# Optimization experiments

Hardware: AMD Instinct MI355X
Metric: run time of the kernel (lower is better)

The kernel has to match this reference:

```python
import jax, jax.numpy as jnp
import numpy as np

H = 64  # hidden size (fixed by module)

def _gru_cell(x, h, Wih, Whh, bih, bhh):
    # PyTorch GRU cell: gates ordered (r, z, n)
    gi = x @ Wih.T + bih            # [B, 3H]
    gh = h @ Whh.T + bhh            # [B, 3H]
    ir, iz, inn = jnp.split(gi, 3, axis=-1)
    hr, hz, hn = jnp.split(gh, 3, axis=-1)
    r = jax.nn.sigmoid(ir + hr)
    z = jax.nn.sigmoid(iz + hz)
    n = jnp.tanh(inn + r * hn)
    return (1.0 - z) * n + z * h


def setup_inputs() -> dict:
    key = jax.random.key(0)
    ks = jax.random.split(key, 24)
    B, T, NI = 16384, 256, 6
    s = 1.0 / np.sqrt(H)  # torch default GRU init scale
    f32 = jnp.float32
    u = lambda k, shp: jax.random.uniform(k, shp, dtype=f32, minval=-s, maxval=s)
    inp = {
        "x": jax.random.normal(ks[0], (B, T, NI), dtype=f32),
        "target_len": 180,
        # encoder GRU, layer 0 (input size NI) and layer 1 (input size H)
        "e_Wih0": u(ks[1], (3 * H, NI)), "e_Whh0": u(ks[2], (3 * H, H)),
        "e_bih0": u(ks[3], (3 * H,)),    "e_bhh0": u(ks[4], (3 * H,)),
        "e_Wih1": u(ks[5], (3 * H, H)),  "e_Whh1": u(ks[6], (3 * H, H)),
        "e_bih1": u(ks[7], (3 * H,)),    "e_bhh1": u(ks[8], (3 * H,)),
        # decoder GRU, layer 0 (input size 1) and layer 1 (input size H)
        "d_Wih0": u(ks[9], (3 * H, 1)),  "d_Whh0": u(ks[10], (3 * H, H)),
        "d_bih0": u(ks[11], (3 * H,)),   "d_bhh0": u(ks[12], (3 * H,)),
        "d_Wih1": u(ks[13], (3 * H, H)), "d_Whh1": u(ks[14], (3 * H, H)),
        "d_bih1": u(ks[15], (3 * H,)),   "d_bhh1": u(ks[16], (3 * H,)),
        # heads
        "W_on": u(ks[17], (1, H)), "b_on": u(ks[18], (1,)),
        "W_cv": u(ks[19], (1, H)), "b_cv": u(ks[20], (1,)),
    }
    return inp


def reference(x, target_len,
              e_Wih0, e_Whh0, e_bih0, e_bhh0, e_Wih1, e_Whh1, e_bih1, e_bhh1,
              d_Wih0, d_Whh0, d_bih0, d_bhh0, d_Wih1, d_Whh1, d_bih1, d_bhh1,
              W_on, b_on, W_cv, b_cv):
    B = x.shape[0]
    on_threshold = 0.5

    # ---- encoder: 2-layer GRU over the input sequence, keep final hidden ----
    def enc_step(carry, xt):
        h0, h1 = carry
        h0 = _gru_cell(xt, h0, e_Wih0, e_Whh0, e_bih0, e_bhh0)
        h1 = _gru_cell(h0, h1, e_Wih1, e_Whh1, e_bih1, e_bhh1)
        return (h0, h1), None

    h_init = (jnp.zeros((B, H), x.dtype), jnp.zeros((B, H), x.dtype))
    (h0, h1), _ = jax.lax.scan(enc_step, h_init, jnp.swapaxes(x, 0, 1))  # [T,B,NI]

    def dec_step(carry, _):
        prev, h0, h1 = carry                                   # prev: [B,1]
        h0 = _gru_cell(prev, h0, d_Wih0, d_Whh0, d_bih0, d_bhh0)
        h1 = _gru_cell(h0, h1, d_Wih1, d_Whh1, d_bih1, d_bhh1)
        cv = h1 @ W_cv.T + b_cv                                # [B,1]
        logit = h1 @ W_on.T + b_on                             # [B,1]
        gated = (jax.nn.sigmoid(logit) > on_threshold).astype(cv.dtype) * cv
        return (gated, h0, h1), gated

    prev0 = jnp.zeros((B, 1), x.dtype)
    _, outs = jax.lax.scan(dec_step, (prev0, h0, h1), None, length=target_len)
    # outs: [target_len, B, 1] -> [B, target_len, 1] (torch.cat along dim=1)
    return jnp.swapaxes(outs, 0, 1)
```

## Files before the change

### kernel.cpp

```cpp
#include <hip/hip_runtime.h>
#include <math.h>

#define TENC 256
#define NIE  6
#define LH   68
#define WSTR 68

__shared__ float sW1[192 * WSTR];
__shared__ float sU1[192 * WSTR];
__shared__ float sHd[132];
__shared__ float sh0[64 * LH];
__shared__ float sh1[64 * LH];

__device__ __forceinline__ float sigm_(float x) { return 1.0f / (1.0f + expf(-x)); }

__device__ __forceinline__ void fma4(float& acc, const float4& a, const float4& b) {
    acc = fmaf(a.x, b.x, acc);
    acc = fmaf(a.y, b.y, acc);
    acc = fmaf(a.z, b.z, acc);
    acc = fmaf(a.w, b.w, acc);
}

__device__ __forceinline__ void stage_w1(const float* __restrict__ W1,
                                         const float* __restrict__ U1) {
    for (int s = threadIdx.x; s < 12288; s += 512) {
        int k = s & 63, row = s >> 6;
        int g = row >> 6, j = row & 63;
        int d = (j * 3 + g) * WSTR + k;
        sW1[d] = W1[s];
        sU1[d] = U1[s];
    }
}

template<int KIN>
__device__ __forceinline__ void layer0_c(const float* __restrict__ U0,
                                         const float* w0r, const float* w0z,
                                         const float* w0n,
                                         const float* xin,
                                         const float* b_r, const float* b_z,
                                         const float* b_nx, const float* b_nh,
                                         int jB, int bl, float hn[2][4])
{
    float ar[2][4], az[2][4], anx[2][4], anh[2][4];
#pragma unroll
    for (int g = 0; g < 4; ++g) {
#pragma unroll
        for (int jj = 0; jj < 2; ++jj) {
            ar[jj][g] = b_r[jj]; az[jj][g] = b_z[jj];
            anx[jj][g] = b_nx[jj]; anh[jj][g] = b_nh[jj];
        }
    }
#pragma unroll
    for (int jj = 0; jj < 2; ++jj)
#pragma unroll
        for (int g = 0; g < 4; ++g)
#pragma unroll
            for (int k = 0; k < KIN; ++k) {
                ar[jj][g]  = fmaf(w0r[jj * KIN + k], xin[g * KIN + k], ar[jj][g]);
                az[jj][g]  = fmaf(w0z[jj * KIN + k], xin[g * KIN + k], az[jj][g]);
                anx[jj][g] = fmaf(w0n[jj * KIN + k], xin[g * KIN + k], anx[jj][g]);
            }
    const float* u0 = U0 + (size_t)jB * 64;
    const float* u1 = U0 + (size_t)(jB + 1) * 64;
    const float* hr0 = sh0 + bl * LH;
#pragma unroll 2
    for (int kc = 0; kc < 64; kc += 4) {
        float4 hv[4];
#pragma unroll
        for (int g = 0; g < 4; ++g)
            hv[g] = *(const float4*)(hr0 + g * (16 * LH) + kc);
        float4 r0 = *(const float4*)(u0 + kc);
        float4 z0 = *(const float4*)(u0 + 4096 + kc);
        float4 n0 = *(const float4*)(u0 + 8192 + kc);
        float4 r1 = *(const float4*)(u1 + kc);
        float4 z1 = *(const float4*)(u1 + 4096 + kc);
        float4 n1 = *(const float4*)(u1 + 8192 + kc);
#pragma unroll
        for (int g = 0; g < 4; ++g) {
            fma4(ar[0][g], r0, hv[g]); fma4(az[0][g], z0, hv[g]); fma4(anh[0][g], n0, hv[g]);
            fma4(ar[1][g], r1, hv[g]); fma4(az[1][g], z1, hv[g]); fma4(anh[1][g], n1, hv[g]);
        }
    }
#pragma unroll
    for (int g = 0; g < 4; ++g) {
        float2 ho = *(const float2*)(sh0 + (bl + 16 * g) * LH + jB);
        float hold[2] = {ho.x, ho.y};
#pragma unroll
        for (int jj = 0; jj < 2; ++jj) {
            float r = sigm_(ar[jj][g]);
            float z = sigm_(az[jj][g]);
            float n = tanhf(fmaf(r, anh[jj][g], anx[jj][g]));
            hn[jj][g] = fmaf(z, hold[jj] - n, n);
        }
    }
}

__device__ __forceinline__ void layer1_c(const float* b_r, const float* b_z,
                                         const float* b_nx, const float* b_nh,
                                         int jB, int bl, float hn[2][4])
{
    float ar[2][4], az[2][4], anx[2][4], anh[2][4];
#pragma unroll
    for (int g = 0; g < 4; ++g) {
#pragma unroll
        for (int jj = 0; jj < 2; ++jj) {
            ar[jj][g] = b_r[jj]; az[jj][g] = b_z[jj];
            anx[jj][g] = b_nx[jj]; anh[jj][g] = b_nh[jj];
        }
    }
    const float* wb0 = sW1 + (jB * 3) * WSTR;
    const float* wb1 = sW1 + ((jB + 1) * 3) * WSTR;
    const float* ub0 = sU1 + (jB * 3) * WSTR;
    const float* ub1 = sU1 + ((jB + 1) * 3) * WSTR;
    const float* xr0 = sh0 + bl * LH;
    const float* hr0 = sh1 + bl * LH;
#pragma unroll 2
    for (int kc = 0; kc < 64; kc += 4) {
        float4 xv[4], hv[4];
#pragma unroll
        for (int g = 0; g < 4; ++g) {
            xv[g] = *(const float4*)(xr0 + g * (16 * LH) + kc);
            hv[g] = *(const float4*)(hr0 + g * (16 * LH) + kc);
        }
        float4 wr0 = *(const float4*)(wb0 + kc);
        float4 wz0 = *(const float4*)(wb0 + WSTR + kc);
        float4 wn0 = *(const float4*)(wb0 + 2 * WSTR + kc);
        float4 ur0 = *(const float4*)(ub0 + kc);
        float4 uz0 = *(const float4*)(ub0 + WSTR + kc);
        float4 un0 = *(const float4*)(ub0 + 2 * WSTR + kc);
        float4 wr1 = *(const float4*)(wb1 + kc);
        float4 wz1 = *(const float4*)(wb1 + WSTR + kc);
        float4 wn1 = *(const float4*)(wb1 + 2 * WSTR + kc);
        float4 ur1 = *(const float4*)(ub1 + kc);
        float4 uz1 = *(const float4*)(ub1 + WSTR + kc);
        float4 un1 = *(const float4*)(ub1 + 2 * WSTR + kc);
#pragma unroll
        for (int g = 0; g < 4; ++g) {
            fma4(ar[0][g], wr0, xv[g]);  fma4(ar[0][g], ur0, hv[g]);
            fma4(az[0][g], wz0, xv[g]);  fma4(az[0][g], uz0, hv[g]);
            fma4(anx[0][g], wn0, xv[g]); fma4(anh[0][g], un0, hv[g]);
            fma4(ar[1][g], wr1, xv[g]);  fma4(ar[1][g], ur1, hv[g]);
            fma4(az[1][g], wz1, xv[g]);  fma4(az[1][g], uz1, hv[g]);
            fma4(anx[1][g], wn1, xv[g]); fma4(anh[1][g], un1, hv[g]);
        }
    }
#pragma unroll
    for (int g = 0; g < 4; ++g) {
        float2 ho = *(const float2*)(sh1 + (bl + 16 * g) * LH + jB);
        float hold[2] = {ho.x, ho.y};
#pragma unroll
        for (int jj = 0; jj < 2; ++jj) {
            float r = sigm_(ar[jj][g]);
            float z = sigm_(az[jj][g]);
            float n = tanhf(fmaf(r, anh[jj][g], anx[jj][g]));
            hn[jj][g] = fmaf(z, hold[jj] - n, n);
        }
    }
}

extern "C" __global__ void __launch_bounds__(512, 2)
ccseq_kernel(const float* __restrict__ x, const int* __restrict__ p_tlen,
             const float* __restrict__ eW0, const float* __restrict__ eU0,
             const float* __restrict__ eBi0, const float* __restrict__ eBh0,
             const float* __restrict__ eW1, const float* __restrict__ eU1,
             const float* __restrict__ eBi1, const float* __restrict__ eBh1,
             const float* __restrict__ dW0, const float* __restrict__ dU0,
             const float* __restrict__ dBi0, const float* __restrict__ dBh0,
             const float* __restrict__ dW1, const float* __restrict__ dU1,
             const float* __restrict__ dBi1, const float* __restrict__ dBh1,
             const float* __restrict__ Won, const float* __restrict__ bon,
             const float* __restrict__ Wcv, const float* __restrict__ bcv,
             float* __restrict__ out)
{
    const int tid  = threadIdx.x;
    const int lane = tid & 63;
    const int wv   = tid >> 6;
    const int jg   = lane >> 4;
    const int bl   = lane & 15;
    const int jB   = wv * 8 + jg * 2;
    const int tlen = p_tlen[0];

    if (tid < 64) { sHd[tid] = Wcv[tid]; sHd[64 + tid] = Won[tid]; }
    for (int i = tid; i < 64 * LH; i += 512) { sh0[i] = 0.0f; sh1[i] = 0.0f; }
    stage_w1(eW1, eU1);
    __syncthreads();

    float w0r[2 * NIE], w0z[2 * NIE], w0n[2 * NIE];
#pragma unroll
    for (int jj = 0; jj < 2; ++jj)
#pragma unroll
        for (int k = 0; k < NIE; ++k) {
            w0r[jj * NIE + k] = eW0[(jB + jj) * NIE + k];
            w0z[jj * NIE + k] = eW0[(64 + jB + jj) * NIE + k];
            w0n[jj * NIE + k] = eW0[(128 + jB + jj) * NIE + k];
        }
    float eb_r[2], eb_z[2], eb_nx[2], eb_nh[2];
    float e1_r[2], e1_z[2], e1_nx[2], e1_nh[2];
#pragma unroll
    for (int jj = 0; jj < 2; ++jj) {
        int j = jB + jj;
        eb_r[jj]  = eBi0[j] + eBh0[j];
        eb_z[jj]  = eBi0[64 + j] + eBh0[64 + j];
        eb_nx[jj] = eBi0[128 + j];
        eb_nh[jj] = eBh0[128 + j];
        e1_r[jj]  = eBi1[j] + eBh1[j];
        e1_z[jj]  = eBi1[64 + j] + eBh1[64 + j];
        e1_nx[jj] = eBi1[128 + j];
        e1_nh[jj] = eBh1[128 + j];
    }

    const size_t bstr = (size_t)TENC * NIE;
    const float* xb[4];
#pragma unroll
    for (int g = 0; g < 4; ++g)
        xb[g] = x + (size_t)(blockIdx.x * 64 + bl + 16 * g) * bstr;

    float xc[4 * NIE], xn[4 * NIE];
#pragma unroll
    for (int g = 0; g < 4; ++g)
#pragma unroll
        for (int k = 0; k < NIE; ++k) xc[g * NIE + k] = xb[g][k];

    for (int t = 0; t < TENC; ++t) {
        const int tn = (t + 1 < TENC) ? (t + 1) : t;
#pragma unroll
        for (int g = 0; g < 4; ++g)
#pragma unroll
            for (int k = 0; k < NIE; ++k) xn[g * NIE + k] = xb[g][tn * NIE + k];

        float hn[2][4];
        layer0_c<NIE>(eU0, w0r, w0z, w0n, xc, eb_r, eb_z, eb_nx, eb_nh, jB, bl, hn);
        __syncthreads();
#pragma unroll
        for (int g = 0; g < 4; ++g)
            *(float2*)(sh0 + (bl + 16 * g) * LH + jB) = make_float2(hn[0][g], hn[1][g]);
        __syncthreads();

        layer1_c(e1_r, e1_z, e1_nx, e1_nh, jB, bl, hn);
        __syncthreads();
#pragma unroll
        for (int g = 0; g < 4; ++g)
            *(float2*)(sh1 + (bl + 16 * g) * LH + jB) = make_float2(hn[0][g], hn[1][g]);
        __syncthreads();

#pragma unroll
        for (int i = 0; i < 4 * NIE; ++i) xc[i] = xn[i];
    }

    stage_w1(dW1, dU1);
    float v0r[2], v0z[2], v0n[2];
    float db_r[2], db_z[2], db_nx[2], db_nh[2];
    float d1_r[2], d1_z[2], d1_nx[2], d1_nh[2];
#pragma unroll
    for (int jj = 0; jj < 2; ++jj) {
        int j = jB + jj;
        v0r[jj] = dW0[j]; v0z[jj] = dW0[64 + j]; v0n[jj] = dW0[128 + j];
        db_r[jj]  = dBi0[j] + dBh0[j];
        db_z[jj]  = dBi0[64 + j] + dBh0[64 + j];
        db_nx[jj] = dBi0[128 + j];
        db_nh[jj] = dBh0[128 + j];
        d1_r[jj]  = dBi1[j] + dBh1[j];
        d1_z[jj]  = dBi1[64 + j] + dBh1[64 + j];
        d1_nx[jj] = dBi1[128 + j];
        d1_nh[jj] = dBh1[128 + j];
    }
    const float hbc = bcv[0], hbo = bon[0];
    __syncthreads();

    float prev[4] = {0.0f, 0.0f, 0.0f, 0.0f};
    for (int t = 0; t < tlen; ++t) {
        float hn[2][4];
        layer0_c<1>(dU0, v0r, v0z, v0n, prev, db_r, db_z, db_nx, db_nh, jB, bl, hn);
        __syncthreads();
#pragma unroll
        for (int g = 0; g < 4; ++g)
            *(float2*)(sh0 + (bl + 16 * g) * LH + jB) = make_float2(hn[0][g], hn[1][g]);
        __syncthreads();

        layer1_c(d1_r, d1_z, d1_nx, d1_nh, jB, bl, hn);
        __syncthreads();
#pragma unroll
        for (int g = 0; g < 4; ++g)
            *(float2*)(sh1 + (bl + 16 * g) * LH + jB) = make_float2(hn[0][g], hn[1][g]);
        __syncthreads();

        float cv[4] = {hbc, hbc, hbc, hbc};
        float lg[4] = {hbo, hbo, hbo, hbo};
        const float* hr0 = sh1 + bl * LH;
#pragma unroll 2
        for (int kc = 0; kc < 64; kc += 4) {
            float4 wc = *(const float4*)(sHd + kc);
            float4 wo = *(const float4*)(sHd + 64 + kc);
#pragma unroll
            for (int g = 0; g < 4; ++g) {
                float4 h4 = *(const float4*)(hr0 + g * (16 * LH) + kc);
                fma4(cv[g], wc, h4);
                fma4(lg[g], wo, h4);
            }
        }
#pragma unroll
        for (int g = 0; g < 4; ++g)
            prev[g] = (lg[g] > 0.0f) ? cv[g] : 0.0f;
        if (tid < 16) {
#pragma unroll
            for (int g = 0; g < 4; ++g)
                out[(size_t)(blockIdx.x * 64 + bl + 16 * g) * tlen + t] = prev[g];
        }
    }
}

extern "C" void kernel_launch(void* const* d_in, const int* in_sizes, int n_in,
                              void* d_out, int out_size, void* d_ws, size_t ws_size,
                              hipStream_t stream)
{
    (void)n_in; (void)out_size; (void)d_ws; (void)ws_size;
    const float* x    = (const float*)d_in[0];
    const int*   tl   = (const int*)d_in[1];
    const float* eW0  = (const float*)d_in[2];
    const float* eU0  = (const float*)d_in[3];
    const float* eBi0 = (const float*)d_in[4];
    const float* eBh0 = (const float*)d_in[5];
    const float* eW1  = (const float*)d_in[6];
    const float* eU1  = (const float*)d_in[7];
    const float* eBi1 = (const float*)d_in[8];
    const float* eBh1 = (const float*)d_in[9];
    const float* dW0  = (const float*)d_in[10];
    const float* dU0  = (const float*)d_in[11];
    const float* dBi0 = (const float*)d_in[12];
    const float* dBh0 = (const float*)d_in[13];
    const float* dW1  = (const float*)d_in[14];
    const float* dU1  = (const float*)d_in[15];
    const float* dBi1 = (const float*)d_in[16];
    const float* dBh1 = (const float*)d_in[17];
    const float* Won  = (const float*)d_in[18];
    const float* bon  = (const float*)d_in[19];
    const float* Wcv  = (const float*)d_in[20];
    const float* bcv  = (const float*)d_in[21];

    const int B    = in_sizes[0] / (TENC * NIE);
    const int nblk = B / 64;

    ccseq_kernel<<<dim3(nblk), dim3(512), 0, stream>>>(
        x, tl, eW0, eU0, eBi0, eBh0, eW1, eU1, eBi1, eBh1,
        dW0, dU0, dBi0, dBh0, dW1, dU1, dBi1, dBh1,
        Won, bon, Wcv, bcv, (float*)d_out);
}
```

Before: 9.665 ms.

## Halve batch per block, stream layer-1 weights from global, double-buffer hidden states

Each block now handles 32 batch rows instead of 64, doubling the grid, and launch bounds target 4 blocks per CU. Layer-1 weights are no longer staged in LDS and are read directly from global/L1 memory. Hidden-state buffers are double-buffered, so each timestep needs two barriers instead of four. This trades per-thread weight reuse (each weight load now feeds only 2 batch rows) and LDS weight locality for higher occupancy and less synchronisation.

```diff
diff --git a/kernel.cpp b/kernel.cpp
--- a/kernel.cpp
+++ b/kernel.cpp
@@ -4,13 +4,11 @@
 #define TENC 256
 #define NIE  6
 #define LH   68
-#define WSTR 68
-
-__shared__ float sW1[192 * WSTR];
-__shared__ float sU1[192 * WSTR];
+#define NB   32
+
 __shared__ float sHd[132];
-__shared__ float sh0[64 * LH];
-__shared__ float sh1[64 * LH];
+__shared__ float sh0[2][NB * LH];
+__shared__ float sh1[2][NB * LH];
 
 __device__ __forceinline__ float sigm_(float x) { return 1.0f / (1.0f + expf(-x)); }
 
@@ -19,17 +17,6 @@
     acc = fmaf(a.y, b.y, acc);
     acc = fmaf(a.z, b.z, acc);
     acc = fmaf(a.w, b.w, acc);
-}
-
-__device__ __forceinline__ void stage_w1(const float* __restrict__ W1,
-                                         const float* __restrict__ U1) {
-    for (int s = threadIdx.x; s < 12288; s += 512) {
-        int k = s & 63, row = s >> 6;
-        int g = row >> 6, j = row & 63;
-        int d = (j * 3 + g) * WSTR + k;
-        sW1[d] = W1[s];
-        sU1[d] = U1[s];
-    }
 }
 
 template<int KIN>
@@ -39,21 +26,22 @@
                                          const float* xin,
                                          const float* b_r, const float* b_z,
                                          const float* b_nx, const float* b_nh,
-                                         int jB, int bl, float hn[2][4])
+                                         int jB, int bl,
+                                         const float* __restrict__ hb,
+                                         float hn[2][2])
 {
-    float ar[2][4], az[2][4], anx[2][4], anh[2][4];
-#pragma unroll
-    for (int g = 0; g < 4; ++g) {
+    float ar[2][2], az[2][2], anx[2][2], anh[2][2];
+#pragma unroll
+    for (int g = 0; g < 2; ++g)
 #pragma unroll
         for (int jj = 0; jj < 2; ++jj) {
             ar[jj][g] = b_r[jj]; az[jj][g] = b_z[jj];
             anx[jj][g] = b_nx[jj]; anh[jj][g] = b_nh[jj];
         }
-    }
 #pragma unroll
     for (int jj = 0; jj < 2; ++jj)
 #pragma unroll
-        for (int g = 0; g < 4; ++g)
+        for (int g = 0; g < 2; ++g)
 #pragma unroll
             for (int k = 0; k < KIN; ++k) {
                 ar[jj][g]  = fmaf(w0r[jj * KIN + k], xin[g * KIN + k], ar[jj][g]);
@@ -62,28 +50,25 @@
             }
     const float* u0 = U0 + (size_t)jB * 64;
     const float* u1 = U0 + (size_t)(jB + 1) * 64;
-    const float* hr0 = sh0 + bl * LH;
+    const float* hr0 = hb + bl * LH;
 #pragma unroll 2
     for (int kc = 0; kc < 64; kc += 4) {
-        float4 hv[4];
-#pragma unroll
-        for (int g = 0; g < 4; ++g)
-            hv[g] = *(const float4*)(hr0 + g * (16 * LH) + kc);
+        float4 hv0 = *(const float4*)(hr0 + kc);
+        float4 hv1 = *(const float4*)(hr0 + 16 * LH + kc);
         float4 r0 = *(const float4*)(u0 + kc);
         float4 z0 = *(const float4*)(u0 + 4096 + kc);
         float4 n0 = *(const float4*)(u0 + 8192 + kc);
         float4 r1 = *(const float4*)(u1 + kc);
         float4 z1 = *(const float4*)(u1 + 4096 + kc);
         float4 n1 = *(const float4*)(u1 + 8192 + kc);
-#pragma unroll
-        for (int g = 0; g < 4; ++g) {
-            fma4(ar[0][g], r0, hv[g]); fma4(az[0][g], z0, hv[g]); fma4(anh[0][g], n0, hv[g]);
-            fma4(ar[1][g], r1, hv[g]); fma4(az[1][g], z1, hv[g]); fma4(anh[1][g], n1, hv[g]);
-        }
-    }
-#pragma unroll
-    for (int g = 0; g < 4; ++g) {
-        float2 ho = *(const float2*)(sh0 + (bl + 16 * g) * LH + jB);
+        fma4(ar[0][0], r0, hv0); fma4(az[0][0], z0, hv0); fma4(anh[0][0], n0, hv0);
+        fma4(ar[1][0], r1, hv0); fma4(az[1][0], z1, hv0); fma4(anh[1][0], n1, hv0);
+        fma4(ar[0][1], r0, hv1); fma4(az[0][1], z0, hv1); fma4(anh[0][1], n0, hv1);
+        fma4(ar[1][1], r1, hv1); fma4(az[1][1], z1, hv1); fma4(anh[1][1], n1, hv1);
+    }
+#pragma unroll
+    for (int g = 0; g < 2; ++g) {
+        float2 ho = *(const float2*)(hb + (bl + 16 * g) * LH + jB);
         float hold[2] = {ho.x, ho.y};
 #pragma unroll
         for (int jj = 0; jj < 2; ++jj) {
@@ -95,58 +80,63 @@
     }
 }
 
-__device__ __forceinline__ void layer1_c(const float* b_r, const float* b_z,
+__device__ __forceinline__ void layer1_c(const float* __restrict__ W1,
+                                         const float* __restrict__ U1,
+                                         const float* b_r, const float* b_z,
                                          const float* b_nx, const float* b_nh,
-                                         int jB, int bl, float hn[2][4])
+                                         int jB, int bl,
+                                         const float* __restrict__ xb,
+                                         const float* __restrict__ hb,
+                                         float hn[2][2])
 {
-    float ar[2][4], az[2][4], anx[2][4], anh[2][4];
-#pragma unroll
-    for (int g = 0; g < 4; ++g) {
+    float ar[2][2], az[2][2], anx[2][2], anh[2][2];
+#pragma unroll
+    for (int g = 0; g < 2; ++g)
 #pragma unroll
         for (int jj = 0; jj < 2; ++jj) {
             ar[jj][g] = b_r[jj]; az[jj][g] = b_z[jj];
             anx[jj][g] = b_nx[jj]; anh[jj][g] = b_nh[jj];
         }
-    }
-    const float* wb0 = sW1 + (jB * 3) * WSTR;
-    const float* wb1 = sW1 + ((jB + 1) * 3) * WSTR;
-    const float* ub0 = sU1 + (jB * 3) * WSTR;
-    const float* ub1 = sU1 + ((jB + 1) * 3) * WSTR;
-    const float* xr0 = sh0 + bl * LH;
-    const float* hr0 = sh1 + bl * LH;
+    const float* w0 = W1 + (size_t)jB * 64;
+    const float* w1 = W1 + (size_t)(jB + 1) * 64;
+    const float* u0 = U1 + (size_t)jB * 64;
+    const float* u1 = U1 + (size_t)(jB + 1) * 64;
+    const float* xr0 = xb + bl * LH;
+    const float* hr0 = hb + bl * LH;
 #pragma unroll 2
     for (int kc = 0; kc < 64; kc += 4) {
-        float4 xv[4], hv[4];
-#pragma unroll
-        for (int g = 0; g < 4; ++g) {
-            xv[g] = *(const float4*)(xr0 + g * (16 * LH) + kc);
-            hv[g] = *(const float4*)(hr0 + g * (16 * LH) + kc);
-        }
-        float4 wr0 = *(const float4*)(wb0 + kc);
-        float4 wz0 = *(const float4*)(wb0 + WSTR + kc);
-        float4 wn0 = *(const float4*)(wb0 + 2 * WSTR + kc);
-        float4 ur0 = *(const float4*)(ub0 + kc);
-        float4 uz0 = *(const float4*)(ub0 + WSTR + kc);
-        float4 un0 = *(const float4*)(ub0 + 2 * WSTR + kc);
-        float4 wr1 = *(const float4*)(wb1 + kc);
-        float4 wz1 = *(const float4*)(wb1 + WSTR + kc);
-        float4 wn1 = *(const float4*)(wb1 + 2 * WSTR + kc);
-        float4 ur1 = *(const float4*)(ub1 + kc);
-        float4 uz1 = *(const float4*)(ub1 + WSTR + kc);
-        float4 un1 = *(const float4*)(ub1 + 2 * WSTR + kc);
-#pragma unroll
-        for (int g = 0; g < 4; ++g) {
-            fma4(ar[0][g], wr0, xv[g]);  fma4(ar[0][g], ur0, hv[g]);
-            fma4(az[0][g], wz0, xv[g]);  fma4(az[0][g], uz0, hv[g]);
-            fma4(anx[0][g], wn0, xv[g]); fma4(anh[0][g], un0, hv[g]);
-            fma4(ar[1][g], wr1, xv[g]);  fma4(ar[1][g], ur1, hv[g]);
-            fma4(az[1][g], wz1, xv[g]);  fma4(az[1][g], uz1, hv[g]);
-            fma4(anx[1][g], wn1, xv[g]); fma4(anh[1][g], un1, hv[g]);
-        }
-    }
-#pragma unroll
-    for (int g = 0; g < 4; ++g) {
-        float2 ho = *(const float2*)(sh1 + (bl + 16 * g) * LH + jB);
+        float4 xv0 = *(const float4*)(xr0 + kc);
+        float4 xv1 = *(const float4*)(xr0 + 16 * LH + kc);
+        float4 hv0 = *(const float4*)(hr0 + kc);
+        float4 hv1 = *(const float4*)(hr0 + 16 * LH + kc);
+        float4 wr0 = *(const float4*)(w0 + kc);
+        float4 wz0 = *(const float4*)(w0 + 4096 + kc);
+        float4 wn0 = *(const float4*)(w0 + 8192 + kc);
+        float4 ur0 = *(const float4*)(u0 + kc);
+        float4 uz0 = *(const float4*)(u0 + 4096 + kc);
+        float4 un0 = *(const float4*)(u0 + 8192 + kc);
+        float4 wr1 = *(const float4*)(w1 + kc);
+        float4 wz1 = *(const float4*)(w1 + 4096 + kc);
+        float4 wn1 = *(const float4*)(w1 + 8192 + kc);
+        float4 ur1 = *(const float4*)(u1 + kc);
+        float4 uz1 = *(const float4*)(u1 + 4096 + kc);
+        float4 un1 = *(const float4*)(u1 + 8192 + kc);
+        fma4(ar[0][0], wr0, xv0);  fma4(ar[0][0], ur0, hv0);
+        fma4(az[0][0], wz0, xv0);  fma4(az[0][0], uz0, hv0);
+        fma4(anx[0][0], wn0, xv0); fma4(anh[0][0], un0, hv0);
+        fma4(ar[1][0], wr1, xv0);  fma4(ar[1][0], ur1, hv0);
+        fma4(az[1][0], wz1, xv0);  fma4(az[1][0], uz1, hv0);
+        fma4(anx[1][0], wn1, xv0); fma4(anh[1][0], un1, hv0);
+        fma4(ar[0][1], wr0, xv1);  fma4(ar[0][1], ur0, hv1);
+        fma4(az[0][1], wz0, xv1);  fma4(az[0][1], uz0, hv1);
+        fma4(anx[0][1], wn0, xv1); fma4(anh[0][1], un0, hv1);
+        fma4(ar[1][1], wr1, xv1);  fma4(ar[1][1], ur1, hv1);
+        fma4(az[1][1], wz1, xv1);  fma4(az[1][1], uz1, hv1);
+        fma4(anx[1][1], wn1, xv1); fma4(anh[1][1], un1, hv1);
+    }
+#pragma unroll
+    for (int g = 0; g < 2; ++g) {
+        float2 ho = *(const float2*)(hb + (bl + 16 * g) * LH + jB);
         float hold[2] = {ho.x, ho.y};
 #pragma unroll
         for (int jj = 0; jj < 2; ++jj) {
@@ -158,7 +148,7 @@
     }
 }
 
-extern "C" __global__ void __launch_bounds__(512, 2)
+extern "C" __global__ void __launch_bounds__(512, 4)
 ccseq_kernel(const float* __restrict__ x, const int* __restrict__ p_tlen,
              const float* __restrict__ eW0, const float* __restrict__ eU0,
              const float* __restrict__ eBi0, const float* __restrict__ eBh0,
@@ -181,8 +171,11 @@
     const int tlen = p_tlen[0];
 
     if (tid < 64) { sHd[tid] = Wcv[tid]; sHd[64 + tid] = Won[tid]; }
-    for (int i = tid; i < 64 * LH; i += 512) { sh0[i] = 0.0f; sh1[i] = 0.0f; }
-    stage_w1(eW1, eU1);
+    {
+        float* z0 = &sh0[0][0];
+        float* z1 = &sh1[0][0];
+        for (int i = tid; i < 2 * NB * LH; i += 512) { z0[i] = 0.0f; z1[i] = 0.0f; }
+    }
     __syncthreads();
 
     float w0r[2 * NIE], w0z[2 * NIE], w0n[2 * NIE];
@@ -210,44 +203,44 @@
     }
 
     const size_t bstr = (size_t)TENC * NIE;
-    const float* xb[4];
-#pragma unroll
-    for (int g = 0; g < 4; ++g)
-        xb[g] = x + (size_t)(blockIdx.x * 64 + bl + 16 * g) * bstr;
-
-    float xc[4 * NIE], xn[4 * NIE];
-#pragma unroll
-    for (int g = 0; g < 4; ++g)
-#pragma unroll
-        for (int k = 0; k < NIE; ++k) xc[g * NIE + k] = xb[g][k];
-
+    const float* xb0 = x + (size_t)(blockIdx.x * NB + bl) * bstr;
+    const float* xb1 = x + (size_t)(blockIdx.x * NB + bl + 16) * bstr;
+
+    float xc[2 * NIE], xn[2 * NIE];
+#pragma unroll
+    for (int k = 0; k < NIE; ++k) { xc[k] = xb0[k]; xc[NIE + k] = xb1[k]; }
+
+    int cur = 0;
     for (int t = 0; t < TENC; ++t) {
         const int tn = (t + 1 < TENC) ? (t + 1) : t;
 #pragma unroll
-        for (int g = 0; g < 4; ++g)
-#pragma unroll
-            for (int k = 0; k < NIE; ++k) xn[g * NIE + k] = xb[g][tn * NIE + k];
-
-        float hn[2][4];
-        layer0_c<NIE>(eU0, w0r, w0z, w0n, xc, eb_r, eb_z, eb_nx, eb_nh, jB, bl, hn);
+        for (int k = 0; k < NIE; ++k) {
+            xn[k]       = xb0[tn * NIE + k];
+            xn[NIE + k] = xb1[tn * NIE + k];
+        }
+
+        float hn[2][2];
+        layer0_c<NIE>(eU0, w0r, w0z, w0n, xc, eb_r, eb_z, eb_nx, eb_nh,
+                      jB, bl, sh0[cur], hn);
+#pragma unroll
+        for (int g = 0; g < 2; ++g)
+            *(float2*)(sh0[cur ^ 1] + (bl + 16 * g) * LH + jB) =
+                make_float2(hn[0][g], hn[1][g]);
         __syncthreads();
-#pragma unroll
-        for (int g = 0; g < 4; ++g)
-            *(float2*)(sh0 + (bl + 16 * g) * LH + jB) = make_float2(hn[0][g], hn[1][g]);
+
+        layer1_c(eW1, eU1, e1_r, e1_z, e1_nx, e1_nh, jB, bl,
+                 sh0[cur ^ 1], sh1[cur], hn);
+#pragma unroll
+        for (int g = 0; g < 2; ++g)
+            *(float2*)(sh1[cur ^ 1] + (bl + 16 * g) * LH + jB) =
+                make_float2(hn[0][g], hn[1][g]);
         __syncthreads();
 
-        layer1_c(e1_r, e1_z, e1_nx, e1_nh, jB, bl, hn);
-        __syncthreads();
-#pragma unroll
-        for (int g = 0; g < 4; ++g)
-            *(float2*)(sh1 + (bl + 16 * g) * LH + jB) = make_float2(hn[0][g], hn[1][g]);
-        __syncthreads();
-
-#pragma unroll
-        for (int i = 0; i < 4 * NIE; ++i) xc[i] = xn[i];
-    }
-
-    stage_w1(dW1, dU1);
+        cur ^= 1;
+#pragma unroll
+        for (int i = 0; i < 2 * NIE; ++i) xc[i] = xn[i];
+    }
+
     float v0r[2], v0z[2], v0n[2];
     float db_r[2], db_z[2], db_nx[2], db_nh[2];
     float d1_r[2], d1_z[2], d1_nx[2], d1_nh[2];
@@ -265,47 +258,46 @@
         d1_nh[jj] = dBh1[128 + j];
     }
     const float hbc = bcv[0], hbo = bon[0];
-    __syncthreads();
-
-    float prev[4] = {0.0f, 0.0f, 0.0f, 0.0f};
+
+    float prev[2] = {0.0f, 0.0f};
     for (int t = 0; t < tlen; ++t) {
-        float hn[2][4];
-        layer0_c<1>(dU0, v0r, v0z, v0n, prev, db_r, db_z, db_nx, db_nh, jB, bl, hn);
+        float hn[2][2];
+        layer0_c<1>(dU0, v0r, v0z, v0n, prev, db_r, db_z, db_nx, db_nh,
+                    jB, bl, sh0[cur], hn);
+#pragma unroll
+        for (int g = 0; g < 2; ++g)
+            *(float2*)(sh0[cur ^ 1] + (bl + 16 * g) * LH + jB) =
+                make_float2(hn[0][g], hn[1][g]);
         __syncthreads();
-#pragma unroll
-        for (int g = 0; g < 4; ++g)
-            *(float2*)(sh0 + (bl + 16 * g) * LH + jB) = make_float2(hn[0][g], hn[1][g]);
+
+        layer1_c(dW1, dU1, d1_r, d1_z, d1_nx, d1_nh, jB, bl,
+                 sh0[cur ^ 1], sh1[cur], hn);
+#pragma unroll
+        for (int g = 0; g < 2; ++g)
+            *(float2*)(sh1[cur ^ 1] + (bl + 16 * g) * LH + jB) =
+                make_float2(hn[0][g], hn[1][g]);
         __syncthreads();
 
-        layer1_c(d1_r, d1_z, d1_nx, d1_nh, jB, bl, hn);
-        __syncthreads();
-#pragma unroll
-        for (int g = 0; g < 4; ++g)
-            *(float2*)(sh1 + (bl + 16 * g) * LH + jB) = make_float2(hn[0][g], hn[1][g]);
-        __syncthreads();
-
-        float cv[4] = {hbc, hbc, hbc, hbc};
-        float lg[4] = {hbo, hbo, hbo, hbo};
-        const float* hr0 = sh1 + bl * LH;
+        float cv[2] = {hbc, hbc};
+        float lg[2] = {hbo, hbo};
+        const float* hr0 = sh1[cur ^ 1] + bl * LH;
 #pragma unroll 2
         for (int kc = 0; kc < 64; kc += 4) {
-            float4 wc = *(const float4*)(sHd + kc);
-            float4 wo = *(const float4*)(sHd + 64 + kc);
-#pragma unroll
-            for (int g = 0; g < 4; ++g) {
-                float4 h4 = *(const float4*)(hr0 + g * (16 * LH) + kc);
-                fma4(cv[g], wc, h4);
-                fma4(lg[g], wo, h4);
-            }
-        }
-#pragma unroll
-        for (int g = 0; g < 4; ++g)
+            float4 wc  = *(const float4*)(sHd + kc);
+            float4 wo  = *(const float4*)(sHd + 64 + kc);
+            float4 h0v = *(const float4*)(hr0 + kc);
+            float4 h1v = *(const float4*)(hr0 + 16 * LH + kc);
+            fma4(cv[0], wc, h0v); fma4(lg[0], wo, h0v);
+            fma4(cv[1], wc, h1v); fma4(lg[1], wo, h1v);
+        }
+#pragma unroll
+        for (int g = 0; g < 2; ++g)
             prev[g] = (lg[g] > 0.0f) ? cv[g] : 0.0f;
         if (tid < 16) {
-#pragma unroll
-            for (int g = 0; g < 4; ++g)
-                out[(size_t)(blockIdx.x * 64 + bl + 16 * g) * tlen + t] = prev[g];
-        }
+            out[(size_t)(blockIdx.x * NB + bl) * tlen + t]      = prev[0];
+            out[(size_t)(blockIdx.x * NB + bl + 16) * tlen + t] = prev[1];
+        }
+        cur ^= 1;
     }
 }
 
@@ -338,7 +330,7 @@
     const float* bcv  = (const float*)d_in[21];
 
     const int B    = in_sizes[0] / (TENC * NIE);
-    const int nblk = B / 64;
+    const int nblk = B / NB;
 
     ccseq_kernel<<<dim3(nblk), dim3(512), 0, stream>>>(
         x, tl, eW0, eU0, eBi0, eBh0, eW1, eU1, eBi1, eBh1,
```

Result: slower. 18.69 ms (+93.3%).
